# Kernel optimization log

Measured on AMD Instinct MI355X. Metric: run time of the kernel, lower is better.

## Reference

```python
import jax, jax.numpy as jnp
import numpy as np

SEG = 8  # conv1d groups


def _grouped_mix(y, W2, b2, seg):
    # y: [b, C_in, L]; W2: [C_out, C_in//seg]; grouped 1x1 conv1d
    b_, cin, L = y.shape
    cout = W2.shape[0]
    yg = y.reshape(b_, seg, cin // seg, L)
    Wg = W2.reshape(seg, cout // seg, cin // seg)
    z = jnp.einsum('bgcl,goc->bgol', yg, Wg).reshape(b_, cout, L)
    return z + b2[None, :, None]


def _mix_h(x, W1, b1, W2, b2):
    # x: [b,h,w,d]
    b_, H, Wd, D = x.shape
    y = jnp.einsum('bhwd,ed->bhwe', x, W1) + b1            # 1x1 conv2d -> [b,h,w,e]
    y = jnp.transpose(y, (0, 3, 1, 2)).reshape(b_, -1, Wd)  # 'b d h w -> b (d h) w'
    z = _grouped_mix(y, W2, b2, SEG)                        # [b, h*h, w]
    attn = jax.nn.softmax(
        z.reshape(b_, H, H, Wd).transpose(0, 3, 1, 2), axis=-1)  # [b,w,h1,h2]
    xr = jnp.transpose(x, (0, 2, 1, 3))                     # [b,w,h,d]
    out = jnp.einsum('bwij,bwjd->bwid', attn, xr)
    return jnp.transpose(out, (0, 2, 1, 3))                 # [b,h,w,d]


def _mix_w(x, W1, b1, W2, b2):
    # x: [b,h,w,d]
    b_, H, Wd, D = x.shape
    y = jnp.einsum('bhwd,ed->bhwe', x, W1) + b1             # [b,h,w,e]
    y = jnp.transpose(y, (0, 3, 2, 1)).reshape(b_, -1, H)   # 'b d w h -> b (d w) h'
    z = _grouped_mix(y, W2, b2, SEG)                        # [b, w*w, h]
    attn = jax.nn.softmax(
        z.reshape(b_, Wd, Wd, H).transpose(0, 3, 1, 2), axis=-1)  # [b,h,w1,w2]
    return jnp.einsum('bhij,bhjd->bhid', attn, x)           # [b,h,w,d]


def setup_inputs() -> dict:
    key = jax.random.key(0)
    ks = jax.random.split(key, 16)
    B, H, W, D, E = 64, 32, 32, 384, 2
    s = 0.05
    return {
        'x':   jax.random.normal(ks[0], (B, H, W, D), jnp.float32),
        'Wc':  jax.random.normal(ks[1], (D, D), jnp.float32) * s,
        'bc':  jnp.zeros((D,), jnp.float32),
        'Wo':  jax.random.normal(ks[2], (D, D), jnp.float32) * s,
        'bo':  jnp.zeros((D,), jnp.float32),
        'W1h': jax.random.normal(ks[3], (E, D), jnp.float32) * s,
        'b1h': jnp.zeros((E,), jnp.float32),
        'W2h': jax.random.normal(ks[4], (H * H, E * H // SEG), jnp.float32) * s,
        'b2h': jnp.zeros((H * H,), jnp.float32),
        'W1w': jax.random.normal(ks[5], (E, D), jnp.float32) * s,
        'b1w': jnp.zeros((E,), jnp.float32),
        'W2w': jax.random.normal(ks[6], (W * W, E * W // SEG), jnp.float32) * s,
        'b2w': jnp.zeros((W * W,), jnp.float32),
    }


def reference(x, Wc, bc, Wo, bo, W1h, b1h, W2h, b2h, W1w, b1w, W2w, b2w):
    Y_c = jnp.einsum('bhwd,od->bhwo', x, Wc) + bc
    Y_h = _mix_h(x, W1h, b1h, W2h, b2h)
    Y_w = _mix_w(x, W1w, b1w, W2w, b2w)
    Y = Y_h + Y_w + Y_c
    return jnp.einsum('bhwd,od->bhwo', Y, Wo) + bo
```

## Files before the change

### kernel.cpp

```cpp
#include <hip/hip_runtime.h>
#include <hip/hip_bf16.h>
#include <cstdint>
#include <cstddef>

typedef __bf16 bf16;
typedef __attribute__((ext_vector_type(8))) __bf16 bf16x8;
typedef __attribute__((ext_vector_type(4))) float floatx4;

#define NPIX 65536

__device__ inline void async_copy16(void* lds, const void* g) {
    __builtin_amdgcn_global_load_lds(
        (const __attribute__((address_space(1))) void*)g,
        (__attribute__((address_space(3))) void*)lds, 16, 0, 0);
}

__global__ void k_prep_w(const float* __restrict__ Wc, const float* __restrict__ bc,
                         const float* __restrict__ Wo, const float* __restrict__ bo,
                         bf16* __restrict__ Wfull, float* __restrict__ bco) {
    int blk = blockIdx.x;
    int t = threadIdx.x;
    if (blk < 384) {
        int o = blk;
        float acc = 0.f;
        for (int d = 0; d < 384; ++d)
            acc += Wo[o * 384 + d] * Wc[d * 384 + t];
        Wfull[(size_t)o * 768 + t]       = (bf16)Wo[o * 384 + t];
        Wfull[(size_t)o * 768 + 384 + t] = (bf16)acc;
    } else {
        int o = t;
        float acc = bo[o];
        for (int d = 0; d < 384; ++d)
            acc += Wo[o * 384 + d] * bc[d];
        bco[o] = acc;
    }
}

__global__ __launch_bounds__(256) void k_proj(const float* __restrict__ xf, bf16* __restrict__ xb,
                       const float* __restrict__ W1h, const float* __restrict__ b1h,
                       const float* __restrict__ W1w, const float* __restrict__ b1w,
                       float* __restrict__ yh, float* __restrict__ yw) {
    __shared__ float Wh[768], Ww[768];
    int t  = threadIdx.x;
    if (t < 192) {
        ((float4*)Wh)[t] = ((const float4*)W1h)[t];
        ((float4*)Ww)[t] = ((const float4*)W1w)[t];
    }
    __syncthreads();
    int lg = t & 7;
    int pg = t >> 3;
    int p  = blockIdx.x * 32 + pg;
    int b = p >> 10, h = (p >> 5) & 31, w = p & 31;
    const float4* xp4 = (const float4*)(xf + (size_t)p * 384);
    float a0 = 0.f, a1 = 0.f, a2 = 0.f, a3 = 0.f;
#pragma unroll
    for (int j = 0; j < 6; ++j) {
        int c = j * 8 + lg;
        float4 xa = xp4[c * 2], xcv = xp4[c * 2 + 1];
        bf16x8 v;
        v[0] = (bf16)xa.x; v[1] = (bf16)xa.y; v[2] = (bf16)xa.z; v[3] = (bf16)xa.w;
        v[4] = (bf16)xcv.x; v[5] = (bf16)xcv.y; v[6] = (bf16)xcv.z; v[7] = (bf16)xcv.w;
        *(bf16x8*)(xb + (size_t)p * 384 + c * 8) = v;
        float4 h0a = *(const float4*)(Wh + c * 8);
        float4 h0b = *(const float4*)(Wh + c * 8 + 4);
        float4 h1a = *(const float4*)(Wh + 384 + c * 8);
        float4 h1b = *(const float4*)(Wh + 384 + c * 8 + 4);
        float4 w0a = *(const float4*)(Ww + c * 8);
        float4 w0b = *(const float4*)(Ww + c * 8 + 4);
        float4 w1a = *(const float4*)(Ww + 384 + c * 8);
        float4 w1b = *(const float4*)(Ww + 384 + c * 8 + 4);
        a0 += xa.x*h0a.x + xa.y*h0a.y + xa.z*h0a.z + xa.w*h0a.w
            + xcv.x*h0b.x + xcv.y*h0b.y + xcv.z*h0b.z + xcv.w*h0b.w;
        a1 += xa.x*h1a.x + xa.y*h1a.y + xa.z*h1a.z + xa.w*h1a.w
            + xcv.x*h1b.x + xcv.y*h1b.y + xcv.z*h1b.z + xcv.w*h1b.w;
        a2 += xa.x*w0a.x + xa.y*w0a.y + xa.z*w0a.z + xa.w*w0a.w
            + xcv.x*w0b.x + xcv.y*w0b.y + xcv.z*w0b.z + xcv.w*w0b.w;
        a3 += xa.x*w1a.x + xa.y*w1a.y + xa.z*w1a.z + xa.w*w1a.w
            + xcv.x*w1b.x + xcv.y*w1b.y + xcv.z*w1b.z + xcv.w*w1b.w;
    }
#pragma unroll
    for (int m = 1; m < 8; m <<= 1) {
        a0 += __shfl_xor(a0, m, 64);
        a1 += __shfl_xor(a1, m, 64);
        a2 += __shfl_xor(a2, m, 64);
        a3 += __shfl_xor(a3, m, 64);
    }
    if (lg == 0) {
        yh[((b * 2 + 0) * 32 + h) * 32 + w] = a0 + b1h[0];
        yh[((b * 2 + 1) * 32 + h) * 32 + w] = a1 + b1h[1];
        yw[((b * 2 + 0) * 32 + w) * 32 + h] = a2 + b1w[0];
        yw[((b * 2 + 1) * 32 + w) * 32 + h] = a3 + b1w[1];
    }
}

__global__ __launch_bounds__(256) void k_attn(const float* __restrict__ yh_in, const float* __restrict__ yw_in,
                       const float* __restrict__ W2h, const float* __restrict__ b2h,
                       const float* __restrict__ W2w, const float* __restrict__ b2w,
                       bf16* __restrict__ attn_h, bf16* __restrict__ attn_w) {
    int blk = blockIdx.x * 4 + (threadIdx.x >> 6);
    const float* yproj; const float* W2; const float* b2; bf16* attn;
    if (blk < 2048) { yproj = yh_in; W2 = W2h; b2 = b2h; attn = attn_h; }
    else            { yproj = yw_in; W2 = W2w; b2 = b2w; attn = attn_w; blk -= 2048; }
    int bi = blk >> 5, r1 = blk & 31;
    int g = r1 >> 2;
    int cb = g * 8;
    int e = cb >> 5, rb = cb & 31;
    int lane = threadIdx.x & 63;
    int l = lane & 31, half = lane >> 5;
    float yv[8];
    const float* ybase = yproj + (((bi * 2 + e) * 32 + rb) * 32 + l);
#pragma unroll
    for (int c = 0; c < 8; ++c) yv[c] = ybase[c * 32];
    float z[16];
#pragma unroll
    for (int jj = 0; jj < 16; ++jj) {
        int r2 = half * 16 + jj;
        int row = r1 * 32 + r2;
        const float4* wp = (const float4*)(W2 + (size_t)row * 8);
        float4 wa = wp[0], wb = wp[1];
        z[jj] = b2[row]
              + yv[0]*wa.x + yv[1]*wa.y + yv[2]*wa.z + yv[3]*wa.w
              + yv[4]*wb.x + yv[5]*wb.y + yv[6]*wb.z + yv[7]*wb.w;
    }
    float m = -1e30f;
#pragma unroll
    for (int jj = 0; jj < 16; ++jj) m = fmaxf(m, z[jj]);
    m = fmaxf(m, __shfl_xor(m, 32, 64));
    float s = 0.f;
#pragma unroll
    for (int jj = 0; jj < 16; ++jj) { z[jj] = __expf(z[jj] - m); s += z[jj]; }
    s += __shfl_xor(s, 32, 64);
    float inv = 1.f / s;
    bf16x8 o0, o1;
#pragma unroll
    for (int jj = 0; jj < 8; ++jj) o0[jj] = (bf16)(z[jj] * inv);
#pragma unroll
    for (int jj = 0; jj < 8; ++jj) o1[jj] = (bf16)(z[8 + jj] * inv);
    bf16x8* dst = (bf16x8*)(attn + ((((size_t)bi * 32 + l) * 32 + r1) * 32 + half * 16));
    dst[0] = o0;
    dst[1] = o1;
}

__global__ __launch_bounds__(256) void k_mix(const bf16* __restrict__ x,
                                             const bf16* __restrict__ attn_h,
                                             const bf16* __restrict__ attn_w,
                                             bf16* __restrict__ T) {
    __shared__ bf16 Xs[1024 * 16];
    __shared__ bf16 Ts[1024 * 16];
    int n = blockIdx.x;
    int a = n >> 5, r = n & 31;
    int q = a * 8 + (r & 7);
    int bi = q / 6, cq = q % 6;
    int c = cq * 4 + (r >> 3);
    int dbase = c * 16;
    int tid = threadIdx.x;
    int wv = tid >> 6, lane = tid & 63;
    int n16 = lane & 15, quad = lane >> 4;

    const char* gbase = (const char*)(x + (size_t)bi * 1024 * 384 + dbase);
#pragma unroll
    for (int it = 0; it < 8; ++it) {
        int p0 = wv * 256 + it * 32;
        const char* g = gbase + (size_t)(p0 + (lane >> 1)) * 768 + (lane & 1) * 16;
        char* l = (char*)Xs + p0 * 32 + lane * 16;
        async_copy16(l, g);
    }
    __syncthreads();

#pragma unroll
    for (int wl = 0; wl < 8; ++wl) {
        int w = wv * 8 + wl;
        const bf16* ab = attn_h + ((size_t)(bi * 32 + w) * 32) * 32;
        bf16x8 af0 = *(const bf16x8*)(ab + n16 * 32 + quad * 8);
        bf16x8 af1 = *(const bf16x8*)(ab + (16 + n16) * 32 + quad * 8);
        bf16x8 bfrag;
#pragma unroll
        for (int i = 0; i < 8; ++i) {
            int j = quad * 8 + i;
            bfrag[i] = Xs[(j * 32 + w) * 16 + n16];
        }
        floatx4 c0 = {0.f, 0.f, 0.f, 0.f}, c1 = {0.f, 0.f, 0.f, 0.f};
        c0 = __builtin_amdgcn_mfma_f32_16x16x32_bf16(af0, bfrag, c0, 0, 0, 0);
        c1 = __builtin_amdgcn_mfma_f32_16x16x32_bf16(af1, bfrag, c1, 0, 0, 0);
#pragma unroll
        for (int rr = 0; rr < 4; ++rr) {
            int h0 = quad * 4 + rr;
            Ts[(h0 * 32 + w) * 16 + n16]        = (bf16)c0[rr];
            Ts[((16 + h0) * 32 + w) * 16 + n16] = (bf16)c1[rr];
        }
    }
    __syncthreads();

#pragma unroll
    for (int hl = 0; hl < 8; ++hl) {
        int h = wv * 8 + hl;
        const bf16* ab = attn_w + ((size_t)(bi * 32 + h) * 32) * 32;
        bf16x8 af0 = *(const bf16x8*)(ab + n16 * 32 + quad * 8);
        bf16x8 af1 = *(const bf16x8*)(ab + (16 + n16) * 32 + quad * 8);
        bf16x8 bfrag;
#pragma unroll
        for (int i = 0; i < 8; ++i) {
            int j = quad * 8 + i;
            bfrag[i] = Xs[(h * 32 + j) * 16 + n16];
        }
        floatx4 c0 = {0.f, 0.f, 0.f, 0.f}, c1 = {0.f, 0.f, 0.f, 0.f};
        c0 = __builtin_amdgcn_mfma_f32_16x16x32_bf16(af0, bfrag, c0, 0, 0, 0);
        c1 = __builtin_amdgcn_mfma_f32_16x16x32_bf16(af1, bfrag, c1, 0, 0, 0);
        bf16* Tr = T + ((size_t)(bi * 32 + h) * 32) * 384 + dbase;
#pragma unroll
        for (int rr = 0; rr < 4; ++rr) {
            int w0 = quad * 4 + rr;
            Tr[(size_t)w0 * 384 + n16] =
                (bf16)(c0[rr] + (float)Ts[(h * 32 + w0) * 16 + n16]);
            Tr[(size_t)(16 + w0) * 384 + n16] =
                (bf16)(c1[rr] + (float)Ts[(h * 32 + 16 + w0) * 16 + n16]);
        }
    }
}

#define LDP 72
__global__ __launch_bounds__(256) void k_gemm(const bf16* __restrict__ T, const bf16* __restrict__ x,
                                              const bf16* __restrict__ Wfull, const float* __restrict__ bco,
                                              float* __restrict__ out) {
    __shared__ bf16 As[128 * LDP];
    __shared__ bf16 Bs[128 * LDP];
    int bx = blockIdx.x;
    int gid = (bx & 7) * 192 + (bx >> 3);
    int nt = gid % 3, pt = gid / 3;
    int obase = nt * 128;
    int pbase = pt * 128;
    int tid = threadIdx.x;
    int wv = tid >> 6, lane = tid & 63;
    int wm = wv & 1, wn = wv >> 1;
    int n16 = lane & 15, quad = lane >> 4;
    int lrow = tid >> 3;
    int lchunk = tid & 7;
    floatx4 zero = {0.f, 0.f, 0.f, 0.f};
    floatx4 acc[4][4];
#pragma unroll
    for (int i = 0; i < 4; ++i)
#pragma unroll
        for (int j = 0; j < 4; ++j) acc[i][j] = zero;

    const bf16* Bg0 = Wfull + (size_t)obase * 768;

    auto load_tile = [&](int kt, bf16x8 (&av)[4], bf16x8 (&bv)[4]) {
        const bf16* Asrc = (kt < 6) ? (T + (size_t)pbase * 384 + kt * 64)
                                    : (x + (size_t)pbase * 384 + (kt - 6) * 64);
        const bf16* Bsrc = Bg0 + kt * 64;
#pragma unroll
        for (int s = 0; s < 4; ++s)
            av[s] = *(const bf16x8*)(Asrc + (size_t)(s * 32 + lrow) * 384 + lchunk * 8);
#pragma unroll
        for (int s = 0; s < 4; ++s)
            bv[s] = *(const bf16x8*)(Bsrc + (size_t)(s * 32 + lrow) * 768 + lchunk * 8);
    };

    auto step = [&](int kt, bf16x8 (&av)[4], bf16x8 (&bv)[4],
                    bf16x8 (&nav)[4], bf16x8 (&nbv)[4]) {
        __syncthreads();
#pragma unroll
        for (int s = 0; s < 4; ++s)
            *(bf16x8*)(As + (s * 32 + lrow) * LDP + lchunk * 8) = av[s];
#pragma unroll
        for (int s = 0; s < 4; ++s)
            *(bf16x8*)(Bs + (s * 32 + lrow) * LDP + lchunk * 8) = bv[s];
        __syncthreads();
        if (kt < 11) load_tile(kt + 1, nav, nbv);
#pragma unroll
        for (int ks = 0; ks < 2; ++ks) {
            bf16x8 a[4], b[4];
#pragma unroll
            for (int i = 0; i < 4; ++i)
                a[i] = *(const bf16x8*)(As + (wm * 64 + i * 16 + n16) * LDP + ks * 32 + quad * 8);
#pragma unroll
            for (int i = 0; i < 4; ++i)
                b[i] = *(const bf16x8*)(Bs + (wn * 64 + i * 16 + n16) * LDP + ks * 32 + quad * 8);
#pragma unroll
            for (int i = 0; i < 4; ++i)
#pragma unroll
                for (int j = 0; j < 4; ++j)
                    acc[i][j] = __builtin_amdgcn_mfma_f32_16x16x32_bf16(a[i], b[j], acc[i][j], 0, 0, 0);
        }
    };

    bf16x8 avA[4], bvA[4], avB[4], bvB[4];
    load_tile(0, avA, bvA);
    for (int kt = 0; kt < 12; kt += 2) {
        step(kt,     avA, bvA, avB, bvB);
        step(kt + 1, avB, bvB, avA, bvA);
    }

#pragma unroll
    for (int j = 0; j < 4; ++j) {
        int o = obase + wn * 64 + j * 16 + n16;
        float bcv = bco[o];
#pragma unroll
        for (int i = 0; i < 4; ++i) {
            int prow = pbase + wm * 64 + i * 16 + quad * 4;
#pragma unroll
            for (int r = 0; r < 4; ++r)
                out[(size_t)(prow + r) * 384 + o] = acc[i][j][r] + bcv;
        }
    }
}

extern "C" void kernel_launch(void* const* d_in, const int* in_sizes, int n_in,
                              void* d_out, int out_size, void* d_ws, size_t ws_size,
                              hipStream_t stream) {
    const float* x   = (const float*)d_in[0];
    const float* Wc  = (const float*)d_in[1];
    const float* bc  = (const float*)d_in[2];
    const float* Wo  = (const float*)d_in[3];
    const float* bo  = (const float*)d_in[4];
    const float* W1h = (const float*)d_in[5];
    const float* b1h = (const float*)d_in[6];
    const float* W2h = (const float*)d_in[7];
    const float* b2h = (const float*)d_in[8];
    const float* W1w = (const float*)d_in[9];
    const float* b1w = (const float*)d_in[10];
    const float* W2w = (const float*)d_in[11];
    const float* b2w = (const float*)d_in[12];
    float* out = (float*)d_out;

    char* ws = (char*)d_ws;
    size_t off = 0;
    auto alloc = [&](size_t bytes) {
        void* p = ws + off;
        off = (off + bytes + 255) & ~(size_t)255;
        return p;
    };
    bf16*  xb     = (bf16*)alloc((size_t)NPIX * 384 * 2);
    float* yh     = (float*)alloc((size_t)131072 * 4);
    float* yw     = (float*)alloc((size_t)131072 * 4);
    bf16*  attn_h = (bf16*)alloc((size_t)2097152 * 2);
    bf16*  attn_w = (bf16*)alloc((size_t)2097152 * 2);
    bf16*  T      = (bf16*)alloc((size_t)NPIX * 384 * 2);
    bf16*  Wfull  = (bf16*)alloc((size_t)384 * 768 * 2);
    float* bco    = (float*)alloc((size_t)384 * 4);

    hipLaunchKernelGGL(k_prep_w, dim3(385), dim3(384), 0, stream, Wc, bc, Wo, bo, Wfull, bco);
    hipLaunchKernelGGL(k_proj, dim3(2048), dim3(256), 0, stream, x, xb, W1h, b1h, W1w, b1w, yh, yw);
    hipLaunchKernelGGL(k_attn, dim3(1024), dim3(256), 0, stream, yh, yw, W2h, b2h, W2w, b2w, attn_h, attn_w);
    hipLaunchKernelGGL(k_mix, dim3(1536), dim3(256), 0, stream, xb, attn_h, attn_w, T);
    hipLaunchKernelGGL(k_gemm, dim3(1536), dim3(256), 0, stream, T, xb, Wfull, bco, out);
}
```

Measured before the change: 317.7 us.

## Fold weight prep into projection kernel and stage attention stores through LDS

The separate weight-precompute kernel is merged into k_proj as 769 extra blocks appended to the grid. This removes one launch and lets the weight folding overlap with the projection work. In k_attn, each block's four waves now write their softmax rows into shared memory. A transposed copy then writes contiguous 256-byte runs to the attention buffer instead of scattered 32-byte stores. The cost is an extra barrier and LDS traffic, and the prep blocks still do a serial 384-long dot product per thread.

```diff
diff --git a/kernel.cpp b/kernel.cpp
--- a/kernel.cpp
+++ b/kernel.cpp
@@ -15,31 +15,36 @@
         (__attribute__((address_space(3))) void*)lds, 16, 0, 0);
 }
 
-__global__ void k_prep_w(const float* __restrict__ Wc, const float* __restrict__ bc,
-                         const float* __restrict__ Wo, const float* __restrict__ bo,
-                         bf16* __restrict__ Wfull, float* __restrict__ bco) {
-    int blk = blockIdx.x;
-    int t = threadIdx.x;
-    if (blk < 384) {
-        int o = blk;
-        float acc = 0.f;
-        for (int d = 0; d < 384; ++d)
-            acc += Wo[o * 384 + d] * Wc[d * 384 + t];
-        Wfull[(size_t)o * 768 + t]       = (bf16)Wo[o * 384 + t];
-        Wfull[(size_t)o * 768 + 384 + t] = (bf16)acc;
-    } else {
-        int o = t;
-        float acc = bo[o];
-        for (int d = 0; d < 384; ++d)
-            acc += Wo[o * 384 + d] * bc[d];
-        bco[o] = acc;
-    }
-}
-
 __global__ __launch_bounds__(256) void k_proj(const float* __restrict__ xf, bf16* __restrict__ xb,
                        const float* __restrict__ W1h, const float* __restrict__ b1h,
                        const float* __restrict__ W1w, const float* __restrict__ b1w,
-                       float* __restrict__ yh, float* __restrict__ yw) {
+                       float* __restrict__ yh, float* __restrict__ yw,
+                       const float* __restrict__ Wc, const float* __restrict__ bc,
+                       const float* __restrict__ Wo, const float* __restrict__ bo,
+                       bf16* __restrict__ Wfull, float* __restrict__ bco) {
+    if (blockIdx.x >= 2048) {
+        int pb = blockIdx.x - 2048;
+        int tid = threadIdx.x;
+        if (pb < 768) {
+            int o = pb >> 1;
+            int t = (pb & 1) * 256 + tid;
+            if (t < 384) {
+                float acc = 0.f;
+                for (int d = 0; d < 384; ++d)
+                    acc += Wo[o * 384 + d] * Wc[d * 384 + t];
+                Wfull[(size_t)o * 768 + t]       = (bf16)Wo[o * 384 + t];
+                Wfull[(size_t)o * 768 + 384 + t] = (bf16)acc;
+            }
+        } else {
+            for (int o = tid; o < 384; o += 256) {
+                float acc = bo[o];
+                for (int d = 0; d < 384; ++d)
+                    acc += Wo[o * 384 + d] * bc[d];
+                bco[o] = acc;
+            }
+        }
+        return;
+    }
     __shared__ float Wh[768], Ww[768];
     int t  = threadIdx.x;
     if (t < 192) {
@@ -97,11 +102,15 @@
                        const float* __restrict__ W2h, const float* __restrict__ b2h,
                        const float* __restrict__ W2w, const float* __restrict__ b2w,
                        bf16* __restrict__ attn_h, bf16* __restrict__ attn_w) {
-    int blk = blockIdx.x * 4 + (threadIdx.x >> 6);
+    __shared__ bf16 Ls[32 * 136];
+    int bx = blockIdx.x;
     const float* yproj; const float* W2; const float* b2; bf16* attn;
-    if (blk < 2048) { yproj = yh_in; W2 = W2h; b2 = b2h; attn = attn_h; }
-    else            { yproj = yw_in; W2 = W2w; b2 = b2w; attn = attn_w; blk -= 2048; }
-    int bi = blk >> 5, r1 = blk & 31;
+    int blk0;
+    if (bx < 512) { yproj = yh_in; W2 = W2h; b2 = b2h; attn = attn_h; blk0 = bx * 4; }
+    else          { yproj = yw_in; W2 = W2w; b2 = b2w; attn = attn_w; blk0 = (bx - 512) * 4; }
+    int bi = blk0 >> 5, r1base = blk0 & 31;
+    int wv = threadIdx.x >> 6;
+    int r1 = r1base + wv;
     int g = r1 >> 2;
     int cb = g * 8;
     int e = cb >> 5, rb = cb & 31;
@@ -136,9 +145,15 @@
     for (int jj = 0; jj < 8; ++jj) o0[jj] = (bf16)(z[jj] * inv);
 #pragma unroll
     for (int jj = 0; jj < 8; ++jj) o1[jj] = (bf16)(z[8 + jj] * inv);
-    bf16x8* dst = (bf16x8*)(attn + ((((size_t)bi * 32 + l) * 32 + r1) * 32 + half * 16));
-    dst[0] = o0;
-    dst[1] = o1;
+    bf16* lp = Ls + l * 136 + wv * 32 + half * 16;
+    *(bf16x8*)lp       = o0;
+    *(bf16x8*)(lp + 8) = o1;
+    __syncthreads();
+    int tl = threadIdx.x >> 3, part = threadIdx.x & 7;
+    const bf16* sp = Ls + tl * 136 + part * 16;
+    bf16* dst = attn + (((size_t)(bi * 32 + tl) * 32 + r1base) * 32) + part * 16;
+    *(bf16x8*)dst       = *(const bf16x8*)sp;
+    *(bf16x8*)(dst + 8) = *(const bf16x8*)(sp + 8);
 }
 
 __global__ __launch_bounds__(256) void k_mix(const bf16* __restrict__ x,
@@ -339,8 +354,9 @@
     bf16*  Wfull  = (bf16*)alloc((size_t)384 * 768 * 2);
     float* bco    = (float*)alloc((size_t)384 * 4);
 
-    hipLaunchKernelGGL(k_prep_w, dim3(385), dim3(384), 0, stream, Wc, bc, Wo, bo, Wfull, bco);
-    hipLaunchKernelGGL(k_proj, dim3(2048), dim3(256), 0, stream, x, xb, W1h, b1h, W1w, b1w, yh, yw);
+    hipLaunchKernelGGL(k_proj, dim3(2048 + 769), dim3(256), 0, stream,
+                       x, xb, W1h, b1h, W1w, b1w, yh, yw,
+                       Wc, bc, Wo, bo, Wfull, bco);
     hipLaunchKernelGGL(k_attn, dim3(1024), dim3(256), 0, stream, yh, yw, W2h, b2h, W2w, b2w, attn_h, attn_w);
     hipLaunchKernelGGL(k_mix, dim3(1536), dim3(256), 0, stream, xb, attn_h, attn_w, T);
     hipLaunchKernelGGL(k_gemm, dim3(1536), dim3(256), 0, stream, T, xb, Wfull, bco, out);
```

Result: no change. 313.1 us (-1.4%).
